# Kernel optimization log

Measured on AMD Instinct MI355X. Metric: run time of the kernel, lower is better.

The kernel has to match this reference:

```python
import jax, jax.numpy as jnp
import numpy as np

N_NODES = 20000
N_EDGES = 320000
HIDDEN = 512
EDGE_DIM = 64
LN_EPS = 1e-5


def mish(x):
    return x * jnp.tanh(jax.nn.softplus(x))


def setup_inputs() -> dict:
    key = jax.random.key(0)
    ks = jax.random.split(key, 8)
    s = lambda fan_in: 1.0 / np.sqrt(fan_in)
    return {
        "x": jax.random.normal(ks[0], (N_NODES, HIDDEN), dtype=jnp.float32),
        "edge_index": jax.random.randint(ks[1], (2, N_EDGES), 0, N_NODES, dtype=jnp.int64),
        "edge_attr": jax.random.normal(ks[2], (N_EDGES, EDGE_DIM), dtype=jnp.float32),
        "W1": jax.random.normal(ks[3], (2 * HIDDEN + EDGE_DIM, HIDDEN), dtype=jnp.float32) * s(2 * HIDDEN + EDGE_DIM),
        "b1": jnp.zeros((HIDDEN,), dtype=jnp.float32),
        "W2": jax.random.normal(ks[4], (HIDDEN, HIDDEN), dtype=jnp.float32) * s(HIDDEN),
        "b2": jnp.zeros((HIDDEN,), dtype=jnp.float32),
        "W3": jax.random.normal(ks[5], (2 * HIDDEN, HIDDEN), dtype=jnp.float32) * s(2 * HIDDEN),
        "b3": jnp.zeros((HIDDEN,), dtype=jnp.float32),
        "W4": jax.random.normal(ks[6], (HIDDEN, HIDDEN), dtype=jnp.float32) * s(HIDDEN),
        "b4": jnp.zeros((HIDDEN,), dtype=jnp.float32),
        "gamma": jnp.ones((HIDDEN,), dtype=jnp.float32),
        "beta": jnp.zeros((HIDDEN,), dtype=jnp.float32),
    }


def reference(x, edge_index, edge_attr, W1, b1, W2, b2, W3, b3, W4, b4, gamma, beta):
    src, dst = edge_index[0], edge_index[1]
    # msg_mlp: Linear -> Mish -> Linear -> Mish on [E, 2H+Edim]
    edge_feat = jnp.concatenate([x[src], x[dst], edge_attr], axis=-1)  # [E, 2H+Edim]
    h = mish(edge_feat @ W1 + b1)
    messages = mish(h @ W2 + b2)  # [E, H]
    # scatter-add messages to destination nodes
    agg = jax.ops.segment_sum(messages, dst, num_segments=x.shape[0])  # [N, H]
    # update_mlp: Linear -> Mish -> Linear
    u = mish(jnp.concatenate([x, agg], axis=-1) @ W3 + b3)
    out = u @ W4 + b4  # [N, H]
    # residual + LayerNorm
    y = x + out
    mu = jnp.mean(y, axis=-1, keepdims=True)
    var = jnp.mean(jnp.square(y - mu), axis=-1, keepdims=True)
    return (y - mu) * jax.lax.rsqrt(var + LN_EPS) * gamma + beta
```

## Files before the change

### kernel.cpp

```cpp
#include <hip/hip_runtime.h>
#include <cstdint>
#include <cstddef>

#define NNODES 20000
#define NEDGES 320000
#define HID 512
#define EDIM 64
#define KFEAT (2*HID + EDIM)

typedef __bf16 bf16x8 __attribute__((ext_vector_type(8)));
typedef short short8 __attribute__((ext_vector_type(8)));
typedef float f32x4 __attribute__((ext_vector_type(4)));

#define AM_NODE 1
#define AM_DIR  2
#define EP_BF16    0
#define EP_F32     2
#define EP_BF16L   3
#define EP_RAW     5

__device__ __forceinline__ uint16_t f2bf(float f){
  uint32_t u = __float_as_uint(f);
  u += 0x7FFFu + ((u >> 16) & 1u);
  return (uint16_t)(u >> 16);
}
__device__ __forceinline__ float bf2f(uint16_t h){
  return __uint_as_float((uint32_t)h << 16);
}
__device__ __forceinline__ float mishf(float v){
  float e = __expf(fminf(v, 18.f));
  float n = e * (e + 2.f);
  return v * __fdividef(n, n + 2.f);
}
__device__ __forceinline__ void gl_lds16(const void* g, void* l){
  __builtin_amdgcn_global_load_lds(
      (const __attribute__((address_space(1))) uint32_t*)g,
      (__attribute__((address_space(3))) uint32_t*)l, 16, 0, 0);
}

__global__ void detect_idx(const int* __restrict__ e, int* __restrict__ flag){
  int i = blockIdx.x * 256 + threadIdx.x;
  if (e[2*i + 1] != 0) atomicOr(flag, 1);
}
__global__ void norm_idx(const int* __restrict__ e, const int* __restrict__ flag,
                         int* __restrict__ s, int* __restrict__ d){
  int i = blockIdx.x * 256 + threadIdx.x;
  if (i >= NEDGES) return;
  int sv, dv;
  if (*flag){ sv = e[i];     dv = e[NEDGES + i]; }
  else      { sv = e[2*i];   dv = e[2*NEDGES + 2*i]; }
  sv = sv < 0 ? 0 : (sv > NNODES-1 ? NNODES-1 : sv);
  dv = dv < 0 ? 0 : (dv > NNODES-1 ? NNODES-1 : dv);
  s[i] = sv; d[i] = dv;
}

__global__ void hist_k(const int* __restrict__ d, int* __restrict__ cnt){
  int i = blockIdx.x * 256 + threadIdx.x;
  if (i < NEDGES) atomicAdd(&cnt[d[i]], 1);
}
__global__ __launch_bounds__(256)
void scan_k(const int* __restrict__ cnt, int* __restrict__ rp, int* __restrict__ cur){
  const int SEG = (NNODES + 255) / 256;
  const int t = threadIdx.x;
  const int lo = t * SEG;
  const int hi = (lo + SEG < NNODES) ? lo + SEG : NNODES;
  int s = 0;
  for (int i = lo; i < hi; ++i) s += cnt[i];
  __shared__ int sh[256];
  sh[t] = s; __syncthreads();
  for (int o = 1; o < 256; o <<= 1){
    int v = (t >= o) ? sh[t - o] : 0;
    __syncthreads();
    sh[t] += v;
    __syncthreads();
  }
  int pre = t ? sh[t-1] : 0;
  for (int i = lo; i < hi; ++i){
    rp[i] = pre; cur[i] = pre; pre += cnt[i];
  }
  if (t == 255) rp[NNODES] = sh[255];
}
__global__ void permute_k(const int* __restrict__ srcN, const int* __restrict__ dstN,
                          int* __restrict__ cur, int* __restrict__ srcS,
                          int* __restrict__ eidx){
  int i = blockIdx.x * 256 + threadIdx.x;
  if (i < NEDGES){
    int d = dstN[i];
    int p = atomicAdd(&cur[d], 1);
    srcS[p] = srcN[i];
    eidx[p] = i;
  }
}
__global__ void fill_dstS(const int* __restrict__ rp, int* __restrict__ dstS){
  int n = blockIdx.x;
  int lo = rp[n], hi = rp[n+1];
  for (int e = lo + threadIdx.x; e < hi; e += 64) dstS[e] = n;
}

__global__ void cast_bf16_vec(const float4* __restrict__ in, ushort4* __restrict__ out, int n4){
  int i = blockIdx.x * 256 + threadIdx.x;
  if (i < n4){
    float4 v = in[i];
    ushort4 o; o.x = f2bf(v.x); o.y = f2bf(v.y); o.z = f2bf(v.z); o.w = f2bf(v.w);
    out[i] = o;
  }
}
__global__ void transpose_cast(const float* __restrict__ W, uint16_t* __restrict__ WT, int K, int N){
  int k = blockIdx.x * 256 + threadIdx.x;
  int n = blockIdx.y;
  if (k < K) WT[(size_t)n * K + k] = f2bf(W[(size_t)k * N + n]);
}

template<int AMODE, int EPI, int KTOT, int BPQ>
__global__ __launch_bounds__(256, 2)
void gemm_k(const uint16_t* __restrict__ A0, const uint16_t* __restrict__ A1,
            const uint16_t* __restrict__ BT, const float* __restrict__ bias,
            uint16_t* __restrict__ Cb, float* __restrict__ Cf,
            int bstr, int cstr, int m0base, int M, int crowOff)
{
  __shared__ __align__(16) char smem[32768];
  char* As = smem;
  char* Bs = smem + 16384;
  const int t = threadIdx.x;
  const int ntx = gridDim.x, nty = gridDim.y;
  int bx = blockIdx.x, by = blockIdx.y;
  if ((nty & 7) == 0){
    int flat = by * ntx + bx;
    int xcd = flat & 7;
    int i = flat >> 3;
    by = xcd * (nty >> 3) + i / ntx;
    bx = i % ntx;
  }
  const int m0 = m0base + by * 128;
  const int n0 = bx * 128;
  const int srow = t >> 3;
  const int c8   = t & 7;
  const int scol = ((c8 ^ (srow & 7)) << 3);
  const int ldst = srow * 128 + c8 * 16;

  const uint16_t* as0[4]; const uint16_t* as1[4];
  #pragma unroll
  for (int i = 0; i < 4; ++i){
    int gm = m0 + srow + 32*i;
    if (gm > M - 1) gm = M - 1;
    if (AMODE == AM_NODE){
      as0[i] = A0 + (size_t)gm * HID;
      as1[i] = A1 + (size_t)gm * HID;
    } else {
      as0[i] = A0 + (size_t)gm * KTOT;
      as1[i] = A0;
    }
  }
  const uint16_t* brow[4];
  #pragma unroll
  for (int i = 0; i < 4; ++i){
    int nr = n0 + srow + 32*i;
    if (BPQ) brow[i] = BT + (size_t)(nr & (HID-1))*bstr + (nr >> 9)*HID;
    else     brow[i] = BT + (size_t)nr*bstr;
  }

  const int lane = t & 63;
  const int wv = t >> 6;
  const int wm = (wv >> 1) * 64;
  const int wn = (wv & 1) * 64;
  const int l15 = lane & 15;
  const int lk16 = (lane >> 4) << 4;
  const int swz = (l15 & 7) << 4;

  f32x4 acc[4][4] = {};

  const int NK = KTOT / 64;
  for (int kk = 0; kk < NK; ++kk){
    const int k0 = kk * 64;
    #pragma unroll
    for (int i = 0; i < 4; ++i){
      const uint16_t* g;
      if (AMODE == AM_NODE){
        g = (k0 < HID) ? as0[i] + (k0 + scol) : as1[i] + (k0 - HID + scol);
      } else {
        g = as0[i] + (k0 + scol);
      }
      gl_lds16(g, As + i*4096 + ldst);
    }
    #pragma unroll
    for (int i = 0; i < 4; ++i)
      gl_lds16(brow[i] + (k0 + scol), Bs + i*4096 + ldst);
    __syncthreads();
    #pragma unroll
    for (int ks = 0; ks < 2; ++ks){
      bf16x8 af[4], bfr[4];
      #pragma unroll
      for (int i = 0; i < 4; ++i){
        const int ar = wm + i*16 + l15;
        af[i] = *(const bf16x8*)(As + ar*128 + ((ks*64 + lk16) ^ swz));
      }
      #pragma unroll
      for (int j = 0; j < 4; ++j){
        const int br = wn + j*16 + l15;
        bfr[j] = *(const bf16x8*)(Bs + br*128 + ((ks*64 + lk16) ^ swz));
      }
      #pragma unroll
      for (int i = 0; i < 4; ++i)
        #pragma unroll
        for (int j = 0; j < 4; ++j)
          acc[i][j] = __builtin_amdgcn_mfma_f32_16x16x32_bf16(af[i], bfr[j], acc[i][j], 0, 0, 0);
    }
    __syncthreads();
  }

  #pragma unroll
  for (int i = 0; i < 4; ++i){
    const int rb = wm + i*16 + ((lane >> 4) << 2);
    #pragma unroll
    for (int j = 0; j < 4; ++j){
      const int gcol = n0 + wn + j*16 + l15;
      const float bv = (EPI == EP_BF16L || EPI == EP_RAW) ? 0.f : bias[gcol];
      #pragma unroll
      for (int r = 0; r < 4; ++r){
        const int grow = m0 + rb + r;
        if (grow < M){
          float v = acc[i][j][r] + bv;
          if (EPI == EP_BF16){
            Cb[(size_t)(grow - crowOff) * cstr + gcol] = f2bf(mishf(v));
          } else if (EPI == EP_BF16L || EPI == EP_RAW){
            Cb[(size_t)(grow - crowOff) * cstr + gcol] = f2bf(v);
          } else {
            Cf[(size_t)grow * cstr + gcol] = v;
          }
        }
      }
    }
  }
}

__global__ __launch_bounds__(256, 4)
void eh_k(const uint16_t* __restrict__ eab, const uint16_t* __restrict__ PQb,
          const int* __restrict__ idx,
          const uint16_t* __restrict__ w1t, const float* __restrict__ b1,
          uint16_t* __restrict__ hb, int m0base, int crowOff)
{
  __shared__ __align__(16) char smem[32768];
  const int t = threadIdx.x;
  const int m0 = m0base + blockIdx.x * 32;
  const int lane = t & 63;
  const int wv = t >> 6;
  const int l15 = lane & 15;
  const int lg = lane >> 4;
  const int* srcS = idx;
  const int* dstS = idx + NEDGES;
  const int* eidx = idx + 2*NEDGES;

  int eidxr[2];
  #pragma unroll
  for (int fr = 0; fr < 2; ++fr) eidxr[fr] = eidx[m0 + fr*16 + l15];

  int sA[8], dA[8];
  #pragma unroll
  for (int it = 0; it < 8; ++it){
    int row2 = (it & 3)*4 + lg;
    int g = m0 + (it >> 2)*16 + row2;
    sA[it] = srcS[g];
    dA[it] = dstS[g];
  }

  const int pqoff = wv*128 + l15*4;
  ushort4 pA0, pA1, qA0, qA1;
  ushort4 pB0, pB1, qB0, qB1;
  auto LDPQ = [&](int s, int d, ushort4& p0, ushort4& p1, ushort4& q0, ushort4& q1){
    const uint16_t* pb = PQb + (size_t)s*1024 + pqoff;
    const uint16_t* qb = PQb + (size_t)d*1024 + 512 + pqoff;
    p0 = *(const ushort4*)pb;  p1 = *(const ushort4*)(pb + 64);
    q0 = *(const ushort4*)qb;  q1 = *(const ushort4*)(qb + 64);
  };
  LDPQ(sA[0], dA[0], pA0, pA1, qA0, qA1);
  LDPQ(sA[1], dA[1], pB0, pB1, qB0, qB1);

  f32x4 acc[2][8] = {};
  #pragma unroll
  for (int ks = 0; ks < 2; ++ks){
    bf16x8 bF[8];
    #pragma unroll
    for (int fc = 0; fc < 8; ++fc){
      int n = wv*128 + fc*16 + l15;
      bF[fc] = *(const bf16x8*)(w1t + (size_t)n*KFEAT + 2*HID + ks*32 + lg*8);
    }
    #pragma unroll
    for (int fr = 0; fr < 2; ++fr){
      bf16x8 av = *(const bf16x8*)(eab + (size_t)eidxr[fr]*EDIM + ks*32 + lg*8);
      #pragma unroll
      for (int fc = 0; fc < 8; ++fc)
        acc[fr][fc] = __builtin_amdgcn_mfma_f32_16x16x32_bf16(av, bF[fc], acc[fr][fc], 0, 0, 0);
    }
  }

  char* slab = smem + wv*8192;
  const float4 b1v0 = *(const float4*)(b1 + wv*128 + l15*4);
  const float4 b1v1 = *(const float4*)(b1 + wv*128 + 64 + l15*4);
  #pragma unroll
  for (int fr = 0; fr < 2; ++fr){
    #pragma unroll
    for (int fc = 0; fc < 8; ++fc){
      #pragma unroll
      for (int r = 0; r < 4; ++r){
        int row = lg*4 + r;
        int cb = ((fc*16 + l15)*4) ^ ((lg & 1) << 6);
        *(float*)(slab + row*512 + cb) = acc[fr][fc][r];
      }
    }
    asm volatile("s_waitcnt lgkmcnt(0)" ::: "memory");
    __builtin_amdgcn_sched_barrier(0);
    #pragma unroll
    for (int i = 0; i < 4; ++i){
      const int it = fr*4 + i;
      ushort4& cp0 = (it & 1) ? pB0 : pA0;
      ushort4& cp1 = (it & 1) ? pB1 : pA1;
      ushort4& cq0 = (it & 1) ? qB0 : qA0;
      ushort4& cq1 = (it & 1) ? qB1 : qA1;
      int row = i*4 + lg;
      int grow = m0 + fr*16 + row;
      float4 v0 = *(const float4*)(slab + row*512 + ((l15*16) ^ ((i & 1) << 6)));
      float4 v1 = *(const float4*)(slab + row*512 + ((256 + l15*16) ^ ((i & 1) << 6)));
      ushort4 h0, h1;
      h0.x = f2bf(mishf(v0.x + bf2f(cp0.x) + bf2f(cq0.x) + b1v0.x));
      h0.y = f2bf(mishf(v0.y + bf2f(cp0.y) + bf2f(cq0.y) + b1v0.y));
      h0.z = f2bf(mishf(v0.z + bf2f(cp0.z) + bf2f(cq0.z) + b1v0.z));
      h0.w = f2bf(mishf(v0.w + bf2f(cp0.w) + bf2f(cq0.w) + b1v0.w));
      h1.x = f2bf(mishf(v1.x + bf2f(cp1.x) + bf2f(cq1.x) + b1v1.x));
      h1.y = f2bf(mishf(v1.y + bf2f(cp1.y) + bf2f(cq1.y) + b1v1.y));
      h1.z = f2bf(mishf(v1.z + bf2f(cp1.z) + bf2f(cq1.z) + b1v1.z));
      h1.w = f2bf(mishf(v1.w + bf2f(cp1.w) + bf2f(cq1.w) + b1v1.w));
      size_t hrow = (size_t)(grow - crowOff) * HID + wv*128;
      *(ushort4*)(hb + hrow + l15*4) = h0;
      *(ushort4*)(hb + hrow + 64 + l15*4) = h1;
      if (it + 2 < 8)
        LDPQ(sA[it+2], dA[it+2], cp0, cp1, cq0, cq1);
    }
    asm volatile("s_waitcnt lgkmcnt(0)" ::: "memory");
    __builtin_amdgcn_sched_barrier(0);
  }
}

__global__ __launch_bounds__(128)
void gather_agg(const uint16_t* __restrict__ msg, const int* __restrict__ rp,
                const float* __restrict__ b2, float* __restrict__ agg,
                uint16_t* __restrict__ aggb, int e0, int e1, int fin){
  const int n = blockIdx.x;
  int lo = rp[n], hi = rp[n+1];
  if (lo < e0) lo = e0;
  if (hi > e1) hi = e1;
  if (!fin && lo >= hi) return;
  const int t = threadIdx.x;
  const float4 bv = ((const float4*)b2)[t];
  float4 a = {0.f, 0.f, 0.f, 0.f};
  for (int e = lo; e < hi; ++e){
    ushort4 m = ((const ushort4*)(msg + (size_t)(e - e0) * HID))[t];
    a.x += mishf(bf2f(m.x) + bv.x);
    a.y += mishf(bf2f(m.y) + bv.y);
    a.z += mishf(bf2f(m.z) + bv.z);
    a.w += mishf(bf2f(m.w) + bv.w);
  }
  float4* ap = ((float4*)(agg + (size_t)n * HID)) + t;
  float4 c = *ap;
  c.x += a.x; c.y += a.y; c.z += a.z; c.w += a.w;
  if (lo < hi) *ap = c;
  if (fin){
    ushort4 o;
    o.x = f2bf(c.x); o.y = f2bf(c.y); o.z = f2bf(c.z); o.w = f2bf(c.w);
    ((ushort4*)(aggb + (size_t)n * HID))[t] = o;
  }
}

__global__ __launch_bounds__(128)
void resid_ln(const float* __restrict__ x, const float* __restrict__ ob,
              const float* __restrict__ gamma, const float* __restrict__ beta,
              float* __restrict__ y){
  const int row = blockIdx.x;
  const int t = threadIdx.x;
  const float4 xv = ((const float4*)(x + (size_t)row * HID))[t];
  const float4 ov = ((const float4*)(ob + (size_t)row * HID))[t];
  float4 s4;
  s4.x = xv.x + ov.x; s4.y = xv.y + ov.y; s4.z = xv.z + ov.z; s4.w = xv.w + ov.w;
  float s = s4.x + s4.y + s4.z + s4.w;
  float q = s4.x*s4.x + s4.y*s4.y + s4.z*s4.z + s4.w*s4.w;
  #pragma unroll
  for (int o = 32; o; o >>= 1){
    s += __shfl_xor(s, o, 64);
    q += __shfl_xor(q, o, 64);
  }
  __shared__ float ss[2], qq[2];
  if ((t & 63) == 0){ ss[t >> 6] = s; qq[t >> 6] = q; }
  __syncthreads();
  const float S = ss[0] + ss[1], Q = qq[0] + qq[1];
  const float mu = S * (1.0f / HID);
  const float var = Q * (1.0f / HID) - mu * mu;
  const float inv = rsqrtf(var + 1e-5f);
  const float4 g = ((const float4*)gamma)[t];
  const float4 b = ((const float4*)beta)[t];
  float4 o;
  o.x = (s4.x - mu) * inv * g.x + b.x;
  o.y = (s4.y - mu) * inv * g.y + b.y;
  o.z = (s4.z - mu) * inv * g.z + b.z;
  o.w = (s4.w - mu) * inv * g.w + b.w;
  ((float4*)(y + (size_t)row * HID))[t] = o;
}

extern "C" void kernel_launch(void* const* d_in, const int* in_sizes, int n_in,
                              void* d_out, int out_size, void* d_ws, size_t ws_size,
                              hipStream_t stream)
{
  const float* x    = (const float*)d_in[0];
  const int*   ei   = (const int*)d_in[1];
  const float* ea   = (const float*)d_in[2];
  const float* W1   = (const float*)d_in[3];
  const float* b1   = (const float*)d_in[4];
  const float* W2   = (const float*)d_in[5];
  const float* b2   = (const float*)d_in[6];
  const float* W3   = (const float*)d_in[7];
  const float* b3   = (const float*)d_in[8];
  const float* W4   = (const float*)d_in[9];
  const float* b4   = (const float*)d_in[10];
  const float* gmm  = (const float*)d_in[11];
  const float* bet  = (const float*)d_in[12];
  float* out = (float*)d_out;

  uint8_t* w = (uint8_t*)d_ws;
  size_t off = 0;
  auto alloc = [&](size_t bytes) -> void* {
    void* p = w + off;
    off += (bytes + 255) & ~(size_t)255;
    return p;
  };
  uint16_t* xb   = (uint16_t*)alloc((size_t)NNODES*HID*2);
  uint16_t* w1t  = (uint16_t*)alloc((size_t)HID*KFEAT*2);
  uint16_t* w2t  = (uint16_t*)alloc((size_t)HID*HID*2);
  uint16_t* w3t  = (uint16_t*)alloc((size_t)HID*1024*2);
  uint16_t* w4t  = (uint16_t*)alloc((size_t)HID*HID*2);
  uint16_t* PQb  = (uint16_t*)alloc((size_t)NNODES*1024*2);
  float*    agg  = (float*)alloc((size_t)NNODES*HID*4);
  float*    outf = (float*)alloc((size_t)NNODES*HID*4);
  int*      srcN = (int*)alloc((size_t)NEDGES*4);
  int*      dstN = (int*)alloc((size_t)NEDGES*4);
  int*      idxS = (int*)alloc((size_t)NEDGES*4*3);
  int*      cnt  = (int*)alloc((size_t)NNODES*4);
  int*      rp   = (int*)alloc((size_t)(NNODES+1)*4);
  int*      cur  = (int*)alloc((size_t)NNODES*4);
  int*      flag = (int*)alloc(256);
  int*      srcS = idxS;
  int*      dstS = idxS + NEDGES;
  int*      eidx = idxS + 2*NEDGES;

  uint16_t* eab  = (uint16_t*)outf;
  uint16_t* aggb = PQb;
  uint16_t* ub   = PQb + (size_t)NNODES*HID;

  size_t remain = (ws_size > off) ? ws_size - off : 0;
  size_t maxChunk = remain / ((size_t)HID*2*2);
  long long chunkE = (long long)(maxChunk & ~(size_t)1023);
  if (chunkE > NEDGES) chunkE = NEDGES;
  if (chunkE < 1024) chunkE = 1024;
  uint16_t* hb   = (uint16_t*)alloc((size_t)chunkE*HID*2);
  uint16_t* msgb = (uint16_t*)alloc((size_t)chunkE*HID*2);

  hipMemsetAsync(agg, 0, (size_t)NNODES*HID*4, stream);
  hipMemsetAsync(cnt, 0, (size_t)NNODES*4, stream);
  hipMemsetAsync(flag, 0, 4, stream);

  detect_idx<<<64, 256, 0, stream>>>(ei, flag);
  norm_idx<<<(NEDGES+255)/256, 256, 0, stream>>>(ei, flag, srcN, dstN);
  hist_k<<<(NEDGES+255)/256, 256, 0, stream>>>(dstN, cnt);
  scan_k<<<1, 256, 0, stream>>>(cnt, rp, cur);
  permute_k<<<(NEDGES+255)/256, 256, 0, stream>>>(srcN, dstN, cur, srcS, eidx);
  fill_dstS<<<NNODES, 64, 0, stream>>>(rp, dstS);

  cast_bf16_vec<<<(NNODES*HID/4+255)/256, 256, 0, stream>>>((const float4*)x, (ushort4*)xb, NNODES*HID/4);
  cast_bf16_vec<<<(NEDGES*EDIM/4+255)/256, 256, 0, stream>>>((const float4*)ea, (ushort4*)eab, NEDGES*EDIM/4);

  transpose_cast<<<dim3((KFEAT+255)/256, HID), 256, 0, stream>>>(W1, w1t, KFEAT, HID);
  transpose_cast<<<dim3((HID+255)/256,   HID), 256, 0, stream>>>(W2, w2t, HID, HID);
  transpose_cast<<<dim3((1024+255)/256,  HID), 256, 0, stream>>>(W3, w3t, 1024, HID);
  transpose_cast<<<dim3((HID+255)/256,   HID), 256, 0, stream>>>(W4, w4t, HID, HID);

  dim3 gpq(1024/128, 160);
  gemm_k<AM_DIR, EP_BF16L, HID, 1><<<gpq, 256, 0, stream>>>(
      xb, nullptr, w1t, b1, PQb, nullptr, KFEAT, 1024, 0, NNODES, 0);

  for (long long e0 = 0; e0 < NEDGES; e0 += chunkE){
    int ce = (int)((NEDGES - e0 < chunkE) ? (NEDGES - e0) : chunkE);
    int fin = (e0 + chunkE >= NEDGES) ? 1 : 0;
    eh_k<<<(ce+31)/32, 256, 0, stream>>>(eab, PQb, idxS, w1t, b1, hb, (int)e0, (int)e0);
    dim3 g2(HID/128, (ce+127)/128);
    gemm_k<AM_DIR, EP_RAW, HID, 0><<<g2, 256, 0, stream>>>(
        hb, nullptr, w2t, b2, msgb, nullptr, HID, HID, 0, ce, 0);
    gather_agg<<<NNODES, 128, 0, stream>>>(msgb, rp, b2, agg, aggb,
                                           (int)e0, (int)(e0+ce), fin);
  }

  dim3 g3(HID/128, 160);
  gemm_k<AM_NODE, EP_BF16, 1024, 0><<<g3, 256, 0, stream>>>(
      xb, aggb, w3t, b3, ub, nullptr, 1024, HID, 0, NNODES, 0);
  gemm_k<AM_DIR, EP_F32, HID, 0><<<g3, 256, 0, stream>>>(
      ub, nullptr, w4t, b4, nullptr, outf, HID, HID, 0, NNODES, 0);

  resid_ln<<<NNODES, 128, 0, stream>>>(x, outf, gmm, bet, out);
}
```

Measured before the change: 913.1 us.

## Parallelize prefix scan, tile weight transpose via LDS, cap edge chunk size

```diff
diff --git a/kernel.cpp b/kernel.cpp
--- a/kernel.cpp
+++ b/kernel.cpp
@@ -7,6 +7,8 @@
 #define HID 512
 #define EDIM 64
 #define KFEAT (2*HID + EDIM)
+#define SB 80
+#define SSEG 250
 
 typedef __bf16 bf16x8 __attribute__((ext_vector_type(8)));
 typedef short short8 __attribute__((ext_vector_type(8)));
@@ -59,26 +61,36 @@
   if (i < NEDGES) atomicAdd(&cnt[d[i]], 1);
 }
 __global__ __launch_bounds__(256)
-void scan_k(const int* __restrict__ cnt, int* __restrict__ rp, int* __restrict__ cur){
-  const int SEG = (NNODES + 255) / 256;
-  const int t = threadIdx.x;
-  const int lo = t * SEG;
-  const int hi = (lo + SEG < NNODES) ? lo + SEG : NNODES;
-  int s = 0;
-  for (int i = lo; i < hi; ++i) s += cnt[i];
+void scan1(const int* __restrict__ cnt, int* __restrict__ rp, int* __restrict__ bsum){
   __shared__ int sh[256];
-  sh[t] = s; __syncthreads();
+  const int b = blockIdx.x, t = threadIdx.x;
+  int v = (t < SSEG) ? cnt[b*SSEG + t] : 0;
+  sh[t] = v; __syncthreads();
   for (int o = 1; o < 256; o <<= 1){
-    int v = (t >= o) ? sh[t - o] : 0;
+    int u = (t >= o) ? sh[t-o] : 0;
     __syncthreads();
-    sh[t] += v;
+    sh[t] += u;
     __syncthreads();
   }
-  int pre = t ? sh[t-1] : 0;
-  for (int i = lo; i < hi; ++i){
-    rp[i] = pre; cur[i] = pre; pre += cnt[i];
-  }
-  if (t == 255) rp[NNODES] = sh[255];
+  if (t < SSEG) rp[b*SSEG + t] = sh[t] - v;
+  if (t == 255) bsum[b] = sh[255];
+}
+__global__ void scan2(const int* __restrict__ bsum, int* __restrict__ boff,
+                      int* __restrict__ rpN){
+  if (threadIdx.x == 0){
+    int acc = 0;
+    for (int i = 0; i < SB; ++i){ boff[i] = acc; acc += bsum[i]; }
+    *rpN = acc;
+  }
+}
+__global__ __launch_bounds__(256)
+void scan3(int* __restrict__ rp, const int* __restrict__ boff, int* __restrict__ cur){
+  const int b = blockIdx.x, t = threadIdx.x;
+  if (t < SSEG){
+    int i = b*SSEG + t;
+    int v = rp[i] + boff[b];
+    rp[i] = v; cur[i] = v;
+  }
 }
 __global__ void permute_k(const int* __restrict__ srcN, const int* __restrict__ dstN,
                           int* __restrict__ cur, int* __restrict__ srcS,
@@ -105,10 +117,24 @@
     out[i] = o;
   }
 }
-__global__ void transpose_cast(const float* __restrict__ W, uint16_t* __restrict__ WT, int K, int N){
-  int k = blockIdx.x * 256 + threadIdx.x;
-  int n = blockIdx.y;
-  if (k < K) WT[(size_t)n * K + k] = f2bf(W[(size_t)k * N + n]);
+__global__ __launch_bounds__(256)
+void transpose_cast(const float* __restrict__ W, uint16_t* __restrict__ WT, int K, int N){
+  __shared__ uint16_t tile[64][65];
+  const int k0 = blockIdx.x * 64;
+  const int n0 = blockIdx.y * 64;
+  const int c = threadIdx.x & 63;
+  const int r0 = threadIdx.x >> 6;
+  #pragma unroll
+  for (int rr = 0; rr < 64; rr += 4){
+    int k = k0 + rr + r0, n = n0 + c;
+    if (k < K && n < N) tile[rr + r0][c] = f2bf(W[(size_t)k*N + n]);
+  }
+  __syncthreads();
+  #pragma unroll
+  for (int rr = 0; rr < 64; rr += 4){
+    int n = n0 + rr + r0, k = k0 + c;
+    if (n < N && k < K) WT[(size_t)n*K + k] = tile[c][rr + r0];
+  }
 }
 
 template<int AMODE, int EPI, int KTOT, int BPQ>
@@ -444,6 +470,8 @@
   int*      cnt  = (int*)alloc((size_t)NNODES*4);
   int*      rp   = (int*)alloc((size_t)(NNODES+1)*4);
   int*      cur  = (int*)alloc((size_t)NNODES*4);
+  int*      bsum = (int*)alloc((size_t)SB*4);
+  int*      boff = (int*)alloc((size_t)SB*4);
   int*      flag = (int*)alloc(256);
   int*      srcS = idxS;
   int*      dstS = idxS + NEDGES;
@@ -456,7 +484,7 @@
   size_t remain = (ws_size > off) ? ws_size - off : 0;
   size_t maxChunk = remain / ((size_t)HID*2*2);
   long long chunkE = (long long)(maxChunk & ~(size_t)1023);
-  if (chunkE > NEDGES) chunkE = NEDGES;
+  if (chunkE > 65536) chunkE = 65536;
   if (chunkE < 1024) chunkE = 1024;
   uint16_t* hb   = (uint16_t*)alloc((size_t)chunkE*HID*2);
   uint16_t* msgb = (uint16_t*)alloc((size_t)chunkE*HID*2);
@@ -468,17 +496,19 @@
   detect_idx<<<64, 256, 0, stream>>>(ei, flag);
   norm_idx<<<(NEDGES+255)/256, 256, 0, stream>>>(ei, flag, srcN, dstN);
   hist_k<<<(NEDGES+255)/256, 256, 0, stream>>>(dstN, cnt);
-  scan_k<<<1, 256, 0, stream>>>(cnt, rp, cur);
+  scan1<<<SB, 256, 0, stream>>>(cnt, rp, bsum);
+  scan2<<<1, 64, 0, stream>>>(bsum, boff, rp + NNODES);
+  scan3<<<SB, 256, 0, stream>>>(rp, boff, cur);
   permute_k<<<(NEDGES+255)/256, 256, 0, stream>>>(srcN, dstN, cur, srcS, eidx);
   fill_dstS<<<NNODES, 64, 0, stream>>>(rp, dstS);
 
   cast_bf16_vec<<<(NNODES*HID/4+255)/256, 256, 0, stream>>>((const float4*)x, (ushort4*)xb, NNODES*HID/4);
   cast_bf16_vec<<<(NEDGES*EDIM/4+255)/256, 256, 0, stream>>>((const float4*)ea, (ushort4*)eab, NEDGES*EDIM/4);
 
-  transpose_cast<<<dim3((KFEAT+255)/256, HID), 256, 0, stream>>>(W1, w1t, KFEAT, HID);
-  transpose_cast<<<dim3((HID+255)/256,   HID), 256, 0, stream>>>(W2, w2t, HID, HID);
-  transpose_cast<<<dim3((1024+255)/256,  HID), 256, 0, stream>>>(W3, w3t, 1024, HID);
-  transpose_cast<<<dim3((HID+255)/256,   HID), 256, 0, stream>>>(W4, w4t, HID, HID);
+  transpose_cast<<<dim3((KFEAT+63)/64, (HID+63)/64), 256, 0, stream>>>(W1, w1t, KFEAT, HID);
+  transpose_cast<<<dim3((HID+63)/64,  (HID+63)/64), 256, 0, stream>>>(W2, w2t, HID, HID);
+  transpose_cast<<<dim3((1024+63)/64, (HID+63)/64), 256, 0, stream>>>(W3, w3t, 1024, HID);
+  transpose_cast<<<dim3((HID+63)/64,  (HID+63)/64), 256, 0, stream>>>(W4, w4t, HID, HID);
 
   dim3 gpq(1024/128, 160);
   gemm_k<AM_DIR, EP_BF16L, HID, 1><<<gpq, 256, 0, stream>>>(
```

Result: no change. 905.5 us (-0.8%).
